# Kernel tuning notes

Hardware: AMD Instinct MI355X
Metric: run time of the kernel (lower is better)

The kernel has to match this reference:

```python
import jax, jax.numpy as jnp
import numpy as np

COMMITMENT_COST = 0.25


def setup_inputs() -> dict:
    key = jax.random.key(0)
    k1, k2 = jax.random.split(key)
    z_e = jax.random.normal(k1, (32, 256, 32, 32), dtype=jnp.float32)
    codebook = jax.random.normal(k2, (1024, 256), dtype=jnp.float32)
    return {"z_e": z_e, "codebook": codebook}


def reference(z_e, codebook):
    B, D, H, W = z_e.shape
    # (B, D, H, W) -> (N, D), N = B*H*W
    z_flat = jnp.transpose(z_e, (0, 2, 3, 1)).reshape(-1, D)
    # squared L2 distances to every codebook entry: (N, K)
    distances = (
        jnp.sum(z_flat * z_flat, axis=1, keepdims=True)
        - 2.0 * (z_flat @ codebook.T)
        + jnp.sum(codebook * codebook, axis=1)
    )
    codes = jnp.argmin(distances, axis=1)          # (N,)
    z_q = jnp.transpose(codebook[codes].reshape(B, H, W, D), (0, 3, 1, 2))
    # straight-through estimator
    z_q_st = z_e + jax.lax.stop_gradient(z_q - z_e)
    codebook_loss = jnp.mean((jax.lax.stop_gradient(z_q) - z_e) ** 2)
    commitment_loss = jnp.mean((z_q - jax.lax.stop_gradient(z_e)) ** 2)
    vq_loss = codebook_loss + COMMITMENT_COST * commitment_loss
    indices = codes.reshape(B, H, W)
    return z_q_st, indices, vq_loss
```

## Files before the change

kernel.cpp:

```cpp
#include <hip/hip_runtime.h>
#include <cstdint>
#include <cstddef>


typedef __attribute__((ext_vector_type(8))) short bf16x8;
typedef __attribute__((ext_vector_type(4))) float f32x4;

#define GL2LDS(g, l) __builtin_amdgcn_global_load_lds( \
    (__attribute__((address_space(1))) const void*)(g), \
    (__attribute__((address_space(3))) void*)(l), 16, 0, 0)

__device__ __forceinline__ unsigned short rne_bf16(float f) {
    unsigned u = __float_as_uint(f);
    return (unsigned short)((u + 0x7FFFu + ((u >> 16) & 1u)) >> 16);
}
__device__ __forceinline__ float bf16_to_f(unsigned short h) {
    return __uint_as_float((unsigned)h << 16);
}

__global__ __launch_bounds__(256)
void vq_cnorm_kernel(const float* __restrict__ cb, float* __restrict__ cnorm)
{
    const int k = blockIdx.x * 256 + threadIdx.x;
    const float4* row = reinterpret_cast<const float4*>(cb + (size_t)k * 256);
    float s0 = 0.f, s1 = 0.f, s2 = 0.f, s3 = 0.f;
#pragma unroll 8
    for (int i = 0; i < 64; ++i) {
        float4 v = row[i];
        s0 = fmaf(v.x, v.x, s0);
        s1 = fmaf(v.y, v.y, s1);
        s2 = fmaf(v.z, v.z, s2);
        s3 = fmaf(v.w, v.w, s3);
    }
    cnorm[k] = (s0 + s1) + (s2 + s3);
}

__global__ __launch_bounds__(256)
void vq_csplit_kernel(const float* __restrict__ cb, unsigned short* __restrict__ c0,
                      unsigned short* __restrict__ c1, unsigned short* __restrict__ c2)
{
    const int idx = blockIdx.x * 256 + threadIdx.x;
    float4 v = reinterpret_cast<const float4*>(cb)[idx];
    float f[4] = { v.x, v.y, v.z, v.w };
    ushort4 h0, h1, h2;
    unsigned short* p0[4] = { &h0.x, &h0.y, &h0.z, &h0.w };
    unsigned short* p1[4] = { &h1.x, &h1.y, &h1.z, &h1.w };
    unsigned short* p2[4] = { &h2.x, &h2.y, &h2.z, &h2.w };
#pragma unroll
    for (int j = 0; j < 4; ++j) {
        unsigned short b0 = rne_bf16(f[j]); float r1 = f[j] - bf16_to_f(b0);
        unsigned short b1 = rne_bf16(r1);   float r2 = r1 - bf16_to_f(b1);
        unsigned short b2 = rne_bf16(r2);
        *p0[j] = b0; *p1[j] = b1; *p2[j] = b2;
    }
    reinterpret_cast<ushort4*>(c0)[idx] = h0;
    reinterpret_cast<ushort4*>(c1)[idx] = h1;
    reinterpret_cast<ushort4*>(c2)[idx] = h2;
}

__global__ __launch_bounds__(256)
void vq_zsplit_kernel(const float* __restrict__ z, unsigned short* __restrict__ z0,
                      unsigned short* __restrict__ z1, unsigned short* __restrict__ z2)
{
    __shared__ float zl[64 * 264];
    const int t = threadIdx.x, blk = blockIdx.x;
    const int b = blk >> 4, hw0 = (blk & 15) << 6;
    const float* zb = z + ((size_t)b << 18) + hw0;
#pragma unroll 8
    for (int i = 0; i < 64; ++i) {
        int idx = i * 256 + t;
        int d = idx >> 6, hwl = idx & 63;
        zl[hwl * 264 + d] = zb[(size_t)d * 1024 + hwl];
    }
    __syncthreads();
    const int n0 = (b << 10) + hw0;
#pragma unroll
    for (int p = 0; p < 8; ++p) {
        const int hwl = p * 8 + (t >> 5);
        const int d0 = (t & 31) * 8;
        const float* src = &zl[hwl * 264 + d0];
        unsigned short h0[8], h1[8], h2[8];
#pragma unroll
        for (int j = 0; j < 8; ++j) {
            float f = src[j];
            unsigned short b0 = rne_bf16(f);  float r1 = f - bf16_to_f(b0);
            unsigned short b1 = rne_bf16(r1); float r2 = r1 - bf16_to_f(b1);
            unsigned short b2 = rne_bf16(r2);
            h0[j] = b0; h1[j] = b1; h2[j] = b2;
        }
        const size_t o = (size_t)(n0 + hwl) * 256 + d0;
        ushort4 a;
        a = ushort4{h0[0],h0[1],h0[2],h0[3]}; *reinterpret_cast<ushort4*>(z0 + o)     = a;
        a = ushort4{h0[4],h0[5],h0[6],h0[7]}; *reinterpret_cast<ushort4*>(z0 + o + 4) = a;
        a = ushort4{h1[0],h1[1],h1[2],h1[3]}; *reinterpret_cast<ushort4*>(z1 + o)     = a;
        a = ushort4{h1[4],h1[5],h1[6],h1[7]}; *reinterpret_cast<ushort4*>(z1 + o + 4) = a;
        a = ushort4{h2[0],h2[1],h2[2],h2[3]}; *reinterpret_cast<ushort4*>(z2 + o)     = a;
        a = ushort4{h2[4],h2[5],h2[6],h2[7]}; *reinterpret_cast<ushort4*>(z2 + o + 4) = a;
    }
}

__global__ __launch_bounds__(512, 2)
void vq_mfma_argmin_kernel(const unsigned short* __restrict__ zp,
                           const unsigned short* __restrict__ cp,
                           const float* __restrict__ cnorm,
                           unsigned long long* __restrict__ packed)
{
    __shared__ unsigned short Ld[2][2][2][256 * 32];

    const int tid = threadIdx.x, l = tid & 63, w = tid >> 6;
    const int wr = w >> 2, wc = w & 3;
    const int nid = ((blockIdx.x & 7) << 6) | (blockIdx.x >> 3);
    const int bm = nid >> 2, bn = nid & 3;
    const int arow = bm * 256, brow = bn * 256;

    f32x4 acc[8][4];
#pragma unroll
    for (int m = 0; m < 8; ++m)
#pragma unroll
        for (int n = 0; n < 4; ++n) acc[m][n] = f32x4{0.f, 0.f, 0.f, 0.f};

    const int srow  = l >> 2;
    const int selem = (((l & 3) ^ ((l >> 3) & 3))) << 3;

    const int lo16 = l & 15, hi4 = l >> 4;
    const int fco = ((hi4 ^ ((lo16 >> 1) & 3))) << 3;

#define STAGE(tt, mat, kk) do {                                               \
    const int seg_ = (tt) >> 2;                                               \
    const unsigned short* S_ = (mat)                                          \
        ? cp + (size_t)((0x211000 >> (seg_ << 2)) & 3) * 262144u              \
        : zp + (size_t)((0x010210 >> (seg_ << 2)) & 3) * 8388608u;            \
    const int R_  = (mat) ? brow : arow;                                      \
    const int KO_ = (((tt) & 3) << 6) + ((kk) << 5) + selem;                  \
    GL2LDS(S_ + (size_t)(R_ + (w * 2 + 0) * 16 + srow) * 256 + KO_,           \
           &Ld[(tt) & 1][mat][kk][(w * 2 + 0) * 512]);                        \
    GL2LDS(S_ + (size_t)(R_ + (w * 2 + 1) * 16 + srow) * 256 + KO_,           \
           &Ld[(tt) & 1][mat][kk][(w * 2 + 1) * 512]);                        \
} while (0)

#define VM12 asm volatile("s_waitcnt vmcnt(12)" ::: "memory")
#define VM8  asm volatile("s_waitcnt vmcnt(8)"  ::: "memory")
#define VM4  asm volatile("s_waitcnt vmcnt(4)"  ::: "memory")
#define VM0  asm volatile("s_waitcnt vmcnt(0)"  ::: "memory")
#define NOPS ((void)0)
#define SBAR do { asm volatile("" ::: "memory");                              \
                  __builtin_amdgcn_s_barrier();                               \
                  __builtin_amdgcn_sched_barrier(0); } while (0)

    bf16x8 bfr0, bfr1, bfr2, bfr3;

#define PH(t, mh, kk, STAGESTMT, VMSTMT) do {                                 \
    const unsigned short* Ap_ = &Ld[(t) & 1][0][kk][0];                       \
    const unsigned short* Bp_ = &Ld[(t) & 1][1][kk][0];                       \
    bf16x8 a0, a1, a2, a3;                                                    \
    a0 = *(const bf16x8*)&Ap_[(wr*128 + ((mh)*4+0)*16 + lo16)*32 + fco];      \
    a1 = *(const bf16x8*)&Ap_[(wr*128 + ((mh)*4+1)*16 + lo16)*32 + fco];      \
    a2 = *(const bf16x8*)&Ap_[(wr*128 + ((mh)*4+2)*16 + lo16)*32 + fco];      \
    a3 = *(const bf16x8*)&Ap_[(wr*128 + ((mh)*4+3)*16 + lo16)*32 + fco];      \
    if ((mh) == 0) {                                                          \
        bfr0 = *(const bf16x8*)&Bp_[(wc*64 + 0*16 + lo16)*32 + fco];          \
        bfr1 = *(const bf16x8*)&Bp_[(wc*64 + 1*16 + lo16)*32 + fco];          \
        bfr2 = *(const bf16x8*)&Bp_[(wc*64 + 2*16 + lo16)*32 + fco];          \
        bfr3 = *(const bf16x8*)&Bp_[(wc*64 + 3*16 + lo16)*32 + fco];          \
    }                                                                         \
    STAGESTMT;                                                                \
    SBAR;                                                                     \
    __builtin_amdgcn_s_setprio(1);                                            \
    acc[(mh)*4+0][0] = __builtin_amdgcn_mfma_f32_16x16x32_bf16(a0, bfr0, acc[(mh)*4+0][0], 0,0,0); \
    acc[(mh)*4+0][1] = __builtin_amdgcn_mfma_f32_16x16x32_bf16(a0, bfr1, acc[(mh)*4+0][1], 0,0,0); \
    acc[(mh)*4+0][2] = __builtin_amdgcn_mfma_f32_16x16x32_bf16(a0, bfr2, acc[(mh)*4+0][2], 0,0,0); \
    acc[(mh)*4+0][3] = __builtin_amdgcn_mfma_f32_16x16x32_bf16(a0, bfr3, acc[(mh)*4+0][3], 0,0,0); \
    acc[(mh)*4+1][0] = __builtin_amdgcn_mfma_f32_16x16x32_bf16(a1, bfr0, acc[(mh)*4+1][0], 0,0,0); \
    acc[(mh)*4+1][1] = __builtin_amdgcn_mfma_f32_16x16x32_bf16(a1, bfr1, acc[(mh)*4+1][1], 0,0,0); \
    acc[(mh)*4+1][2] = __builtin_amdgcn_mfma_f32_16x16x32_bf16(a1, bfr2, acc[(mh)*4+1][2], 0,0,0); \
    acc[(mh)*4+1][3] = __builtin_amdgcn_mfma_f32_16x16x32_bf16(a1, bfr3, acc[(mh)*4+1][3], 0,0,0); \
    acc[(mh)*4+2][0] = __builtin_amdgcn_mfma_f32_16x16x32_bf16(a2, bfr0, acc[(mh)*4+2][0], 0,0,0); \
    acc[(mh)*4+2][1] = __builtin_amdgcn_mfma_f32_16x16x32_bf16(a2, bfr1, acc[(mh)*4+2][1], 0,0,0); \
    acc[(mh)*4+2][2] = __builtin_amdgcn_mfma_f32_16x16x32_bf16(a2, bfr2, acc[(mh)*4+2][2], 0,0,0); \
    acc[(mh)*4+2][3] = __builtin_amdgcn_mfma_f32_16x16x32_bf16(a2, bfr3, acc[(mh)*4+2][3], 0,0,0); \
    acc[(mh)*4+3][0] = __builtin_amdgcn_mfma_f32_16x16x32_bf16(a3, bfr0, acc[(mh)*4+3][0], 0,0,0); \
    acc[(mh)*4+3][1] = __builtin_amdgcn_mfma_f32_16x16x32_bf16(a3, bfr1, acc[(mh)*4+3][1], 0,0,0); \
    acc[(mh)*4+3][2] = __builtin_amdgcn_mfma_f32_16x16x32_bf16(a3, bfr2, acc[(mh)*4+3][2], 0,0,0); \
    acc[(mh)*4+3][3] = __builtin_amdgcn_mfma_f32_16x16x32_bf16(a3, bfr3, acc[(mh)*4+3][3], 0,0,0); \
    __builtin_amdgcn_s_setprio(0);                                            \
    VMSTMT;                                                                   \
    SBAR;                                                                     \
} while (0)

#define TILE(t, SA0, SB0, SA1, SB1, V2, V4)                                   \
    PH(t, 0, 0, SA0, NOPS);                                                   \
    PH(t, 1, 0, SB0, V2);                                                     \
    PH(t, 0, 1, SA1, NOPS);                                                   \
    PH(t, 1, 1, SB1, V4)

    STAGE(0, 0, 0); STAGE(0, 1, 0); STAGE(0, 0, 1); STAGE(0, 1, 1);
    STAGE(1, 0, 0); STAGE(1, 1, 0); STAGE(1, 0, 1); STAGE(1, 1, 1);
    VM12;
    SBAR;

    TILE(0, NOPS, NOPS, NOPS, NOPS, VM8, VM4);
#pragma unroll 2
    for (int t = 1; t <= 22; ++t) {
        TILE(t, STAGE(t + 1, 0, 0), STAGE(t + 1, 1, 0),
                STAGE(t + 1, 0, 1), STAGE(t + 1, 1, 1), VM4, VM4);
    }
    TILE(23, NOPS, NOPS, NOPS, NOPS, VM0, NOPS);

#undef TILE
#undef PH
#undef STAGE

    int coln[4]; float cnv[4];
#pragma unroll
    for (int n = 0; n < 4; ++n) {
        coln[n] = brow + wc * 64 + n * 16 + lo16;
        cnv[n] = cnorm[coln[n]];
    }
#pragma unroll
    for (int m = 0; m < 8; ++m) {
#pragma unroll
        for (int j = 0; j < 4; ++j) {
            unsigned long long best = 0xFFFFFFFFFFFFFFFFull;
#pragma unroll
            for (int n = 0; n < 4; ++n) {
                float d = fmaf(-2.0f, acc[m][n][j], cnv[n]);
                unsigned u = __float_as_uint(d);
                u = (u & 0x80000000u) ? ~u : (u | 0x80000000u);
                unsigned long long pk = ((unsigned long long)u << 32) | (unsigned)coln[n];
                best = pk < best ? pk : best;
            }
#pragma unroll
            for (int mask = 1; mask <= 8; mask <<= 1) {
                unsigned long long o = __shfl_xor(best, mask, 64);
                best = o < best ? o : best;
            }
            if (lo16 == 0) {
                const int row = arow + wr * 128 + m * 16 + hi4 * 4 + j;
                atomicMin(&packed[row], best);
            }
        }
    }
}

__global__ __launch_bounds__(256, 2)
void vq_gather_packed_kernel(const float* __restrict__ cb, const float* __restrict__ z,
                             const unsigned long long* __restrict__ packed,
                             float* __restrict__ out_zq, float* __restrict__ out_idx,
                             float* __restrict__ loss)
{
    __shared__ float rows[64 * 257];
    __shared__ int   ks[64];
    __shared__ float wsum[4];

    const int t   = threadIdx.x;
    const int blk = blockIdx.x;
    const int b   = blk >> 4;
    const int hw0 = (blk & 15) << 6;
    const int n0  = blk << 6;

    if (t < 64) {
        const int k = (int)(packed[n0 + t] & 0xFFFFFFFFull);
        ks[t] = k;
        out_idx[n0 + t] = (float)k;
    }
    __syncthreads();

#pragma unroll 4
    for (int i = 0; i < 64; ++i) {
        rows[i * 257 + t] = cb[(size_t)ks[i] * 256 + t];
    }
    __syncthreads();

    const int dq = t >> 6;
    const int hw = t & 63;
    const size_t obase = ((size_t)b << 18) + hw0 + hw;
    float sum = 0.f;
#pragma unroll 4
    for (int dd = 0; dd < 64; ++dd) {
        const int d = (dq << 6) + dd;
        const float  q  = rows[hw * 257 + d];
        const size_t a  = obase + (size_t)d * 1024;
        const float  zv = z[a];
        out_zq[a] = q;
        const float diff = q - zv;
        sum = fmaf(diff, diff, sum);
    }
#pragma unroll
    for (int m = 1; m <= 32; m <<= 1) sum += __shfl_xor(sum, m, 64);
    if ((t & 63) == 0) wsum[t >> 6] = sum;
    __syncthreads();
    if (t == 0) {
        const float s = (wsum[0] + wsum[1]) + (wsum[2] + wsum[3]);
        atomicAdd(loss, s * (1.25f / 8388608.0f));
    }
}

__global__ __launch_bounds__(256)
void vq_transpose_kernel(const float* __restrict__ cb, float* __restrict__ ctT)
{
    __shared__ float tile[64 * 65];
    const int t  = threadIdx.x;
    const int kb = blockIdx.x >> 2, db = blockIdx.x & 3;
    const int k0 = kb << 6, d0 = db << 6;
#pragma unroll
    for (int i = 0; i < 16; ++i) {
        int idx = i * 256 + t;
        int r = idx >> 6, c = idx & 63;
        tile[r * 65 + c] = cb[(size_t)(k0 + r) * 256 + d0 + c];
    }
    __syncthreads();
#pragma unroll
    for (int i = 0; i < 16; ++i) {
        int idx = i * 256 + t;
        int r = idx >> 6, c = idx & 63;
        ctT[(size_t)(d0 + r) * 1024 + k0 + c] = tile[c * 65 + r];
    }
}

__global__ __launch_bounds__(512, 2)
void vq_argmin_kernel(const float* __restrict__ z, const float* __restrict__ ctT,
                      const float* __restrict__ cnorm, int* __restrict__ codes,
                      float* __restrict__ out_idx)
{
    __shared__ float zt[256 * 64];
    __shared__ float ct[16 * 256];
    const int t = threadIdx.x, tx = t & 63, ty = t >> 6, p0 = ty << 3;
    const int blk = blockIdx.x, b = blk >> 4, hw0 = (blk & 15) << 6;
    const float* zbase = z + ((size_t)b << 18) + hw0;
#pragma unroll
    for (int i = 0; i < 8; ++i) {
        int idx = i * 512 + t;
        int d = idx >> 4, c4 = (idx & 15) << 2;
        float4 v = *reinterpret_cast<const float4*>(zbase + (size_t)d * 1024 + c4);
        *reinterpret_cast<float4*>(&zt[d * 64 + c4]) = v;
    }
    float minv[8]; int mini[8];
#pragma unroll
    for (int i = 0; i < 8; ++i) { minv[i] = 3.0e38f; mini[i] = 0; }
    const float* zrd = &zt[p0];
    const float* crd = &ct[tx << 2];
    for (int kt = 0; kt < 4; ++kt) {
        const int k0 = kt << 8;
        float acc[8][4];
#pragma unroll
        for (int i = 0; i < 8; ++i)
#pragma unroll
            for (int j = 0; j < 4; ++j) acc[i][j] = 0.f;
        for (int dc = 0; dc < 16; ++dc) {
            const int d0 = dc << 4;
            __syncthreads();
#pragma unroll
            for (int i = 0; i < 2; ++i) {
                int idx = i * 512 + t;
                int r = idx >> 6, c4 = (idx & 63) << 2;
                float4 v = *reinterpret_cast<const float4*>(ctT + (size_t)(d0 + r) * 1024 + k0 + c4);
                *reinterpret_cast<float4*>(&ct[r * 256 + c4]) = v;
            }
            __syncthreads();
            const float* zp = zrd + d0 * 64;
#pragma unroll
            for (int d = 0; d < 16; ++d) {
                float4 za = *reinterpret_cast<const float4*>(zp + d * 64);
                float4 zb = *reinterpret_cast<const float4*>(zp + d * 64 + 4);
                float4 cc = *reinterpret_cast<const float4*>(crd + d * 256);
#define VQ_FMA_ROW(ii, zv)                          \
                acc[ii][0] = fmaf(zv, cc.x, acc[ii][0]); \
                acc[ii][1] = fmaf(zv, cc.y, acc[ii][1]); \
                acc[ii][2] = fmaf(zv, cc.z, acc[ii][2]); \
                acc[ii][3] = fmaf(zv, cc.w, acc[ii][3]);
                VQ_FMA_ROW(0, za.x) VQ_FMA_ROW(1, za.y) VQ_FMA_ROW(2, za.z) VQ_FMA_ROW(3, za.w)
                VQ_FMA_ROW(4, zb.x) VQ_FMA_ROW(5, zb.y) VQ_FMA_ROW(6, zb.z) VQ_FMA_ROW(7, zb.w)
#undef VQ_FMA_ROW
            }
        }
#pragma unroll
        for (int j = 0; j < 4; ++j) {
            const int k = k0 + (tx << 2) + j;
            const float cn = cnorm[k];
#pragma unroll
            for (int i = 0; i < 8; ++i) {
                float dist = fmaf(-2.0f, acc[i][j], cn);
                if (dist < minv[i]) { minv[i] = dist; mini[i] = k; }
            }
        }
    }
#pragma unroll
    for (int m = 1; m <= 32; m <<= 1) {
#pragma unroll
        for (int i = 0; i < 8; ++i) {
            float ov = __shfl_xor(minv[i], m, 64);
            int   oi = __shfl_xor(mini[i], m, 64);
            if (ov < minv[i] || (ov == minv[i] && oi < mini[i])) { minv[i] = ov; mini[i] = oi; }
        }
    }
    if (tx == 0) {
        const int n0 = (blk << 6) + p0;
#pragma unroll
        for (int i = 0; i < 8; ++i) {
            codes[n0 + i]   = mini[i];
            out_idx[n0 + i] = (float)mini[i];
        }
    }
}

__global__ __launch_bounds__(256, 2)
void vq_gather_kernel(const float* __restrict__ cb, const float* __restrict__ z,
                      const int* __restrict__ codes, float* __restrict__ out_zq,
                      float* __restrict__ loss)
{
    __shared__ float rows[64 * 257];
    __shared__ int   ks[64];
    __shared__ float wsum[4];
    const int t = threadIdx.x, blk = blockIdx.x;
    const int b = blk >> 4, hw0 = (blk & 15) << 6, n0 = blk << 6;
    if (t < 64) ks[t] = codes[n0 + t];
    __syncthreads();
#pragma unroll 4
    for (int i = 0; i < 64; ++i) rows[i * 257 + t] = cb[(size_t)ks[i] * 256 + t];
    __syncthreads();
    const int dq = t >> 6, hw = t & 63;
    const size_t obase = ((size_t)b << 18) + hw0 + hw;
    float sum = 0.f;
#pragma unroll 4
    for (int dd = 0; dd < 64; ++dd) {
        const int d = (dq << 6) + dd;
        const float  q  = rows[hw * 257 + d];
        const size_t a  = obase + (size_t)d * 1024;
        const float  zv = z[a];
        out_zq[a] = q;
        const float diff = q - zv;
        sum = fmaf(diff, diff, sum);
    }
#pragma unroll
    for (int m = 1; m <= 32; m <<= 1) sum += __shfl_xor(sum, m, 64);
    if ((t & 63) == 0) wsum[t >> 6] = sum;
    __syncthreads();
    if (t == 0) {
        const float s = (wsum[0] + wsum[1]) + (wsum[2] + wsum[3]);
        atomicAdd(loss, s * (1.25f / 8388608.0f));
    }
}

extern "C" void kernel_launch(void* const* d_in, const int* in_sizes, int n_in,
                              void* d_out, int out_size, void* d_ws, size_t ws_size,
                              hipStream_t stream)
{
    (void)in_sizes; (void)n_in; (void)out_size;

    const float* z  = (const float*)d_in[0];
    const float* cb = (const float*)d_in[1];

    float* out      = (float*)d_out;
    float* out_zq   = out;
    float* out_idx  = out + 8388608;
    float* out_loss = out + 8421376;

    const size_t NEED = 262144ull + 3ull * 16777216ull + 3ull * 524288ull + 4096ull;

    if (ws_size >= NEED) {
        unsigned long long* packed = (unsigned long long*)d_ws;
        unsigned short* z0 = (unsigned short*)((char*)d_ws + 262144);
        unsigned short* z1 = z0 + 8388608u;
        unsigned short* z2 = z1 + 8388608u;
        unsigned short* c0 = z2 + 8388608u;
        unsigned short* c1 = c0 + 262144u;
        unsigned short* c2 = c1 + 262144u;
        float* cnorm = (float*)(c2 + 262144u);

        hipMemsetAsync(out_loss, 0, sizeof(float), stream);
        hipMemsetAsync(packed, 0xFF, 262144, stream);
        vq_csplit_kernel<<<256, 256, 0, stream>>>(cb, c0, c1, c2);
        vq_cnorm_kernel<<<4, 256, 0, stream>>>(cb, cnorm);
        vq_zsplit_kernel<<<512, 256, 0, stream>>>(z, z0, z1, z2);
        vq_mfma_argmin_kernel<<<512, 512, 0, stream>>>(z0, c0, cnorm, packed);
        vq_gather_packed_kernel<<<512, 256, 0, stream>>>(cb, z, packed, out_zq, out_idx, out_loss);
    } else {
        float* ctT   = (float*)d_ws;
        float* cnorm = ctT + 256 * 1024;
        int*   codes = (int*)(cnorm + 1024);

        hipMemsetAsync(out_loss, 0, sizeof(float), stream);
        vq_transpose_kernel<<<64, 256, 0, stream>>>(cb, ctT);
        vq_cnorm_kernel<<<4, 256, 0, stream>>>(cb, cnorm);
        vq_argmin_kernel<<<512, 512, 0, stream>>>(z, ctT, cnorm, codes, out_idx);
        vq_gather_kernel<<<512, 256, 0, stream>>>(cb, z, codes, out_zq, out_loss);
    }
}
```

Baseline: 155.6 us.

## Restructure MFMA pipeline into two-phase tiles with shallower prefetch and single-wave occupancy

Each tile's inner loop is cut from four phases (half M per phase) to two phases that load all eight A fragments and four B fragments at once and issue 32 MFMAs per barrier pair. The prefetch depth drops from two tiles ahead to one, and launch bounds change to one block per CU so the compiler can use more registers. The aim is to halve the number of barriers and improve MFMA issue density. The cost is lower occupancy and less load latency hidden by the shallower prefetch.

```diff
diff --git a/kernel.cpp b/kernel.cpp
--- a/kernel.cpp
+++ b/kernel.cpp
@@ -99,7 +99,7 @@
     }
 }
 
-__global__ __launch_bounds__(512, 2)
+__global__ __launch_bounds__(512, 1)
 void vq_mfma_argmin_kernel(const unsigned short* __restrict__ zp,
                            const unsigned short* __restrict__ cp,
                            const float* __restrict__ cnorm,
@@ -138,8 +138,6 @@
            &Ld[(tt) & 1][mat][kk][(w * 2 + 1) * 512]);                        \
 } while (0)
 
-#define VM12 asm volatile("s_waitcnt vmcnt(12)" ::: "memory")
-#define VM8  asm volatile("s_waitcnt vmcnt(8)"  ::: "memory")
 #define VM4  asm volatile("s_waitcnt vmcnt(4)"  ::: "memory")
 #define VM0  asm volatile("s_waitcnt vmcnt(0)"  ::: "memory")
 #define NOPS ((void)0)
@@ -147,67 +145,78 @@
                   __builtin_amdgcn_s_barrier();                               \
                   __builtin_amdgcn_sched_barrier(0); } while (0)
 
-    bf16x8 bfr0, bfr1, bfr2, bfr3;
-
-#define PH(t, mh, kk, STAGESTMT, VMSTMT) do {                                 \
+#define PH2(t, kk, STAGESTMT, VMSTMT) do {                                    \
     const unsigned short* Ap_ = &Ld[(t) & 1][0][kk][0];                       \
     const unsigned short* Bp_ = &Ld[(t) & 1][1][kk][0];                       \
-    bf16x8 a0, a1, a2, a3;                                                    \
-    a0 = *(const bf16x8*)&Ap_[(wr*128 + ((mh)*4+0)*16 + lo16)*32 + fco];      \
-    a1 = *(const bf16x8*)&Ap_[(wr*128 + ((mh)*4+1)*16 + lo16)*32 + fco];      \
-    a2 = *(const bf16x8*)&Ap_[(wr*128 + ((mh)*4+2)*16 + lo16)*32 + fco];      \
-    a3 = *(const bf16x8*)&Ap_[(wr*128 + ((mh)*4+3)*16 + lo16)*32 + fco];      \
-    if ((mh) == 0) {                                                          \
-        bfr0 = *(const bf16x8*)&Bp_[(wc*64 + 0*16 + lo16)*32 + fco];          \
-        bfr1 = *(const bf16x8*)&Bp_[(wc*64 + 1*16 + lo16)*32 + fco];          \
-        bfr2 = *(const bf16x8*)&Bp_[(wc*64 + 2*16 + lo16)*32 + fco];          \
-        bfr3 = *(const bf16x8*)&Bp_[(wc*64 + 3*16 + lo16)*32 + fco];          \
-    }                                                                         \
+    bf16x8 a0 = *(const bf16x8*)&Ap_[(wr*128 + 0*16 + lo16)*32 + fco];        \
+    bf16x8 a1 = *(const bf16x8*)&Ap_[(wr*128 + 1*16 + lo16)*32 + fco];        \
+    bf16x8 a2 = *(const bf16x8*)&Ap_[(wr*128 + 2*16 + lo16)*32 + fco];        \
+    bf16x8 a3 = *(const bf16x8*)&Ap_[(wr*128 + 3*16 + lo16)*32 + fco];        \
+    bf16x8 a4 = *(const bf16x8*)&Ap_[(wr*128 + 4*16 + lo16)*32 + fco];        \
+    bf16x8 a5 = *(const bf16x8*)&Ap_[(wr*128 + 5*16 + lo16)*32 + fco];        \
+    bf16x8 a6 = *(const bf16x8*)&Ap_[(wr*128 + 6*16 + lo16)*32 + fco];        \
+    bf16x8 a7 = *(const bf16x8*)&Ap_[(wr*128 + 7*16 + lo16)*32 + fco];        \
+    bf16x8 b0 = *(const bf16x8*)&Bp_[(wc*64 + 0*16 + lo16)*32 + fco];         \
+    bf16x8 b1 = *(const bf16x8*)&Bp_[(wc*64 + 1*16 + lo16)*32 + fco];         \
+    bf16x8 b2 = *(const bf16x8*)&Bp_[(wc*64 + 2*16 + lo16)*32 + fco];         \
+    bf16x8 b3 = *(const bf16x8*)&Bp_[(wc*64 + 3*16 + lo16)*32 + fco];         \
     STAGESTMT;                                                                \
     SBAR;                                                                     \
     __builtin_amdgcn_s_setprio(1);                                            \
-    acc[(mh)*4+0][0] = __builtin_amdgcn_mfma_f32_16x16x32_bf16(a0, bfr0, acc[(mh)*4+0][0], 0,0,0); \
-    acc[(mh)*4+0][1] = __builtin_amdgcn_mfma_f32_16x16x32_bf16(a0, bfr1, acc[(mh)*4+0][1], 0,0,0); \
-    acc[(mh)*4+0][2] = __builtin_amdgcn_mfma_f32_16x16x32_bf16(a0, bfr2, acc[(mh)*4+0][2], 0,0,0); \
-    acc[(mh)*4+0][3] = __builtin_amdgcn_mfma_f32_16x16x32_bf16(a0, bfr3, acc[(mh)*4+0][3], 0,0,0); \
-    acc[(mh)*4+1][0] = __builtin_amdgcn_mfma_f32_16x16x32_bf16(a1, bfr0, acc[(mh)*4+1][0], 0,0,0); \
-    acc[(mh)*4+1][1] = __builtin_amdgcn_mfma_f32_16x16x32_bf16(a1, bfr1, acc[(mh)*4+1][1], 0,0,0); \
-    acc[(mh)*4+1][2] = __builtin_amdgcn_mfma_f32_16x16x32_bf16(a1, bfr2, acc[(mh)*4+1][2], 0,0,0); \
-    acc[(mh)*4+1][3] = __builtin_amdgcn_mfma_f32_16x16x32_bf16(a1, bfr3, acc[(mh)*4+1][3], 0,0,0); \
-    acc[(mh)*4+2][0] = __builtin_amdgcn_mfma_f32_16x16x32_bf16(a2, bfr0, acc[(mh)*4+2][0], 0,0,0); \
-    acc[(mh)*4+2][1] = __builtin_amdgcn_mfma_f32_16x16x32_bf16(a2, bfr1, acc[(mh)*4+2][1], 0,0,0); \
-    acc[(mh)*4+2][2] = __builtin_amdgcn_mfma_f32_16x16x32_bf16(a2, bfr2, acc[(mh)*4+2][2], 0,0,0); \
-    acc[(mh)*4+2][3] = __builtin_amdgcn_mfma_f32_16x16x32_bf16(a2, bfr3, acc[(mh)*4+2][3], 0,0,0); \
-    acc[(mh)*4+3][0] = __builtin_amdgcn_mfma_f32_16x16x32_bf16(a3, bfr0, acc[(mh)*4+3][0], 0,0,0); \
-    acc[(mh)*4+3][1] = __builtin_amdgcn_mfma_f32_16x16x32_bf16(a3, bfr1, acc[(mh)*4+3][1], 0,0,0); \
-    acc[(mh)*4+3][2] = __builtin_amdgcn_mfma_f32_16x16x32_bf16(a3, bfr2, acc[(mh)*4+3][2], 0,0,0); \
-    acc[(mh)*4+3][3] = __builtin_amdgcn_mfma_f32_16x16x32_bf16(a3, bfr3, acc[(mh)*4+3][3], 0,0,0); \
+    acc[0][0] = __builtin_amdgcn_mfma_f32_16x16x32_bf16(a0, b0, acc[0][0], 0,0,0); \
+    acc[0][1] = __builtin_amdgcn_mfma_f32_16x16x32_bf16(a0, b1, acc[0][1], 0,0,0); \
+    acc[0][2] = __builtin_amdgcn_mfma_f32_16x16x32_bf16(a0, b2, acc[0][2], 0,0,0); \
+    acc[0][3] = __builtin_amdgcn_mfma_f32_16x16x32_bf16(a0, b3, acc[0][3], 0,0,0); \
+    acc[1][0] = __builtin_amdgcn_mfma_f32_16x16x32_bf16(a1, b0, acc[1][0], 0,0,0); \
+    acc[1][1] = __builtin_amdgcn_mfma_f32_16x16x32_bf16(a1, b1, acc[1][1], 0,0,0); \
+    acc[1][2] = __builtin_amdgcn_mfma_f32_16x16x32_bf16(a1, b2, acc[1][2], 0,0,0); \
+    acc[1][3] = __builtin_amdgcn_mfma_f32_16x16x32_bf16(a1, b3, acc[1][3], 0,0,0); \
+    acc[2][0] = __builtin_amdgcn_mfma_f32_16x16x32_bf16(a2, b0, acc[2][0], 0,0,0); \
+    acc[2][1] = __builtin_amdgcn_mfma_f32_16x16x32_bf16(a2, b1, acc[2][1], 0,0,0); \
+    acc[2][2] = __builtin_amdgcn_mfma_f32_16x16x32_bf16(a2, b2, acc[2][2], 0,0,0); \
+    acc[2][3] = __builtin_amdgcn_mfma_f32_16x16x32_bf16(a2, b3, acc[2][3], 0,0,0); \
+    acc[3][0] = __builtin_amdgcn_mfma_f32_16x16x32_bf16(a3, b0, acc[3][0], 0,0,0); \
+    acc[3][1] = __builtin_amdgcn_mfma_f32_16x16x32_bf16(a3, b1, acc[3][1], 0,0,0); \
+    acc[3][2] = __builtin_amdgcn_mfma_f32_16x16x32_bf16(a3, b2, acc[3][2], 0,0,0); \
+    acc[3][3] = __builtin_amdgcn_mfma_f32_16x16x32_bf16(a3, b3, acc[3][3], 0,0,0); \
+    acc[4][0] = __builtin_amdgcn_mfma_f32_16x16x32_bf16(a4, b0, acc[4][0], 0,0,0); \
+    acc[4][1] = __builtin_amdgcn_mfma_f32_16x16x32_bf16(a4, b1, acc[4][1], 0,0,0); \
+    acc[4][2] = __builtin_amdgcn_mfma_f32_16x16x32_bf16(a4, b2, acc[4][2], 0,0,0); \
+    acc[4][3] = __builtin_amdgcn_mfma_f32_16x16x32_bf16(a4, b3, acc[4][3], 0,0,0); \
+    acc[5][0] = __builtin_amdgcn_mfma_f32_16x16x32_bf16(a5, b0, acc[5][0], 0,0,0); \
+    acc[5][1] = __builtin_amdgcn_mfma_f32_16x16x32_bf16(a5, b1, acc[5][1], 0,0,0); \
+    acc[5][2] = __builtin_amdgcn_mfma_f32_16x16x32_bf16(a5, b2, acc[5][2], 0,0,0); \
+    acc[5][3] = __builtin_amdgcn_mfma_f32_16x16x32_bf16(a5, b3, acc[5][3], 0,0,0); \
+    acc[6][0] = __builtin_amdgcn_mfma_f32_16x16x32_bf16(a6, b0, acc[6][0], 0,0,0); \
+    acc[6][1] = __builtin_amdgcn_mfma_f32_16x16x32_bf16(a6, b1, acc[6][1], 0,0,0); \
+    acc[6][2] = __builtin_amdgcn_mfma_f32_16x16x32_bf16(a6, b2, acc[6][2], 0,0,0); \
+    acc[6][3] = __builtin_amdgcn_mfma_f32_16x16x32_bf16(a6, b3, acc[6][3], 0,0,0); \
+    acc[7][0] = __builtin_amdgcn_mfma_f32_16x16x32_bf16(a7, b0, acc[7][0], 0,0,0); \
+    acc[7][1] = __builtin_amdgcn_mfma_f32_16x16x32_bf16(a7, b1, acc[7][1], 0,0,0); \
+    acc[7][2] = __builtin_amdgcn_mfma_f32_16x16x32_bf16(a7, b2, acc[7][2], 0,0,0); \
+    acc[7][3] = __builtin_amdgcn_mfma_f32_16x16x32_bf16(a7, b3, acc[7][3], 0,0,0); \
     __builtin_amdgcn_s_setprio(0);                                            \
     VMSTMT;                                                                   \
     SBAR;                                                                     \
 } while (0)
 
-#define TILE(t, SA0, SB0, SA1, SB1, V2, V4)                                   \
-    PH(t, 0, 0, SA0, NOPS);                                                   \
-    PH(t, 1, 0, SB0, V2);                                                     \
-    PH(t, 0, 1, SA1, NOPS);                                                   \
-    PH(t, 1, 1, SB1, V4)
+#define TILE2(t, S0, S1, V1, V2)                                              \
+    PH2(t, 0, S0, V1);                                                        \
+    PH2(t, 1, S1, V2)
 
     STAGE(0, 0, 0); STAGE(0, 1, 0); STAGE(0, 0, 1); STAGE(0, 1, 1);
-    STAGE(1, 0, 0); STAGE(1, 1, 0); STAGE(1, 0, 1); STAGE(1, 1, 1);
-    VM12;
+    VM4;
     SBAR;
 
-    TILE(0, NOPS, NOPS, NOPS, NOPS, VM8, VM4);
 #pragma unroll 2
-    for (int t = 1; t <= 22; ++t) {
-        TILE(t, STAGE(t + 1, 0, 0), STAGE(t + 1, 1, 0),
-                STAGE(t + 1, 0, 1), STAGE(t + 1, 1, 1), VM4, VM4);
-    }
-    TILE(23, NOPS, NOPS, NOPS, NOPS, VM0, NOPS);
-
-#undef TILE
-#undef PH
+    for (int t = 0; t <= 22; ++t) {
+        TILE2(t, { STAGE(t + 1, 0, 0); STAGE(t + 1, 1, 0); },
+                 { STAGE(t + 1, 0, 1); STAGE(t + 1, 1, 1); }, VM4, VM4);
+    }
+    TILE2(23, NOPS, NOPS, VM0, NOPS);
+
+#undef TILE2
+#undef PH2
 #undef STAGE
 
     int coln[4]; float cnv[4];
```

New measurement: 188.5 us. 21.1% more time.
